# Performance work log

Measured on AMD Instinct MI355X. Metric: run time of the kernel, lower is better.

## Reference

```python
import jax, jax.numpy as jnp
import numpy as np

R = 4  # search_range

def setup_inputs() -> dict:
    key = jax.random.key(0)
    k1, k2 = jax.random.split(key)
    B, C, H, W = 4, 128, 96, 160
    src = jax.random.normal(k1, (B, C, H, W), dtype=jnp.float32)
    tgt = jax.random.normal(k2, (B, C, H, W), dtype=jnp.float32)
    return {"src": src, "tgt": tgt}

def _cost_volume(src, tgt):
    B, C, H, W = src.shape
    # zero-pad tgt by R on each spatial side (as in F.pad(tgt, [R]*4))
    tp = jnp.pad(tgt, ((0, 0), (0, 0), (R, R), (R, R)))
    # shifted map cropped to the central HxW window; shift (dh, dw) means
    # the neighbor at offset (dh, dw) relative to each src pixel.
    def crop(dh, dw):
        return tp[:, :, R + dh:R + dh + H, R + dw:R + dw + W]
    # order matches torch: [identity, left, right, up, down] for i=1..R
    maps = [crop(0, 0)]
    for i in range(1, R + 1):
        maps.extend([crop(-i, 0), crop(i, 0), crop(0, -i), crop(0, i)])
    neigh = jnp.stack(maps, axis=2)  # [B, C, 1+4R, H, W]
    # correlation: sum over channels -> [B, 1+4R, H, W]
    return jnp.einsum('bchw,bcshw->bshw', src, neigh)

def reference(src, tgt):
    return _cost_volume(src, tgt)
```

## Files before the change

### kernel.cpp

```cpp
#include <hip/hip_runtime.h>

#define RR 4
#define NS 17
#define BB 4
#define CC 128
#define HH 96
#define WW 160
#define HWSZ (HH * WW)

#define TW 32
#define HTILE 8
#define TROWS (HTILE + 2 * RR)
#define TCOLS (TW + 2 * RR)
#define TILE_E (TROWS * TCOLS)
#define CCHUNK 32
#define NCHUNK (CC / CCHUNK)
#define CG 8
#define NG (CCHUNK / CG)
#define NSPX (WW / TW)
#define NSPY (HH / HTILE)
#define NSP (NSPX * NSPY)
#define NWG (NSP * BB * NCHUNK)
#define NXCD 8
#define WGPX (NWG / NXCD)

#define FMA4S(a, t, s0, s1, s2, s3) \
    (a) = fmaf((s0), (t).x, fmaf((s1), (t).y, fmaf((s2), (t).z, fmaf((s3), (t).w, (a)))))

__global__ __launch_bounds__(256, 4)
void cost_volume_kernel(const float* __restrict__ src,
                        const float* __restrict__ tgt,
                        float* __restrict__ out) {
    __shared__ float4 tileA[TILE_E];
    __shared__ float4 tileB[TILE_E];

    const int x   = threadIdx.x;
    const int hg  = threadIdx.y;
    const int tid = hg * TW + x;

    const int flat = blockIdx.x;
    const int wg   = (flat & (NXCD - 1)) * WGPX + (flat >> 3);
    const int sp   = wg % NSP;
    const int z    = wg / NSP;
    const int wx   = sp % NSPX;
    const int wy   = sp / NSPX;

    const int w0 = wx * TW;
    const int h0 = wy * HTILE;
    const int b  = z & 3;
    const int c0 = (z >> 2) * CCHUNK;

    const int w = w0 + x;
    const int h = h0 + hg;

    const float* tgt_b = tgt + (size_t)(b * CC + c0) * HWSZ;
    const float* src_p = src + (size_t)(b * CC + c0) * HWSZ + h * WW + w;

    int  sOff[3];
    bool sVal[3];
#pragma unroll
    for (int k = 0; k < 3; ++k) {
        const int idx = tid + k * 256;
        const int r   = idx / TCOLS;
        const int col = idx - r * TCOLS;
        const int gr  = h0 - RR + r;
        const int gc  = w0 - RR + col;
        sVal[k] = (idx < TILE_E) && gr >= 0 && gr < HH && gc >= 0 && gc < WW;
        sOff[k] = gr * WW + gc;
    }

    float4 prA[3], prB[3];
    float  sv8[8];

    auto fetch = [&](int g) {
        const float* t = tgt_b + (size_t)(g * CG) * HWSZ;
#pragma unroll
        for (int k = 0; k < 3; ++k) {
            float4 va = make_float4(0.f, 0.f, 0.f, 0.f);
            float4 vb = make_float4(0.f, 0.f, 0.f, 0.f);
            if (sVal[k]) {
                const float* p = t + sOff[k];
                va.x = p[0];
                va.y = p[HWSZ];
                va.z = p[2 * HWSZ];
                va.w = p[3 * HWSZ];
                vb.x = p[4 * HWSZ];
                vb.y = p[5 * HWSZ];
                vb.z = p[6 * HWSZ];
                vb.w = p[7 * HWSZ];
            }
            prA[k] = va;
            prB[k] = vb;
        }
        const float* s = src_p + (size_t)(g * CG) * HWSZ;
#pragma unroll
        for (int k = 0; k < 8; ++k) sv8[k] = s[k * HWSZ];
    };

    float acc[NS];
#pragma unroll
    for (int s = 0; s < NS; ++s) acc[s] = 0.f;

    fetch(0);
    const int base = (RR + hg) * TCOLS + (RR + x);

    for (int g = 0; g < NG; ++g) {
        tileA[tid]       = prA[0];
        tileA[tid + 256] = prA[1];
        if (tid + 512 < TILE_E) tileA[tid + 512] = prA[2];
        tileB[tid]       = prB[0];
        tileB[tid + 256] = prB[1];
        if (tid + 512 < TILE_E) tileB[tid + 512] = prB[2];
        const float a0 = sv8[0], a1 = sv8[1], a2 = sv8[2], a3 = sv8[3];
        const float b0 = sv8[4], b1 = sv8[5], b2 = sv8[6], b3 = sv8[7];
        __syncthreads();

        if (g + 1 < NG) fetch(g + 1);

        {
            float4 tc = tileA[base];
            FMA4S(acc[0], tc, a0, a1, a2, a3);
#pragma unroll
            for (int off = 1; off <= RR; ++off) {
                float4 tu = tileA[base - off * TCOLS];
                float4 td = tileA[base + off * TCOLS];
                float4 tl = tileA[base - off];
                float4 tr = tileA[base + off];
                FMA4S(acc[4 * off - 3], tu, a0, a1, a2, a3);
                FMA4S(acc[4 * off - 2], td, a0, a1, a2, a3);
                FMA4S(acc[4 * off - 1], tl, a0, a1, a2, a3);
                FMA4S(acc[4 * off    ], tr, a0, a1, a2, a3);
            }
            float4 uc = tileB[base];
            FMA4S(acc[0], uc, b0, b1, b2, b3);
#pragma unroll
            for (int off = 1; off <= RR; ++off) {
                float4 tu = tileB[base - off * TCOLS];
                float4 td = tileB[base + off * TCOLS];
                float4 tl = tileB[base - off];
                float4 tr = tileB[base + off];
                FMA4S(acc[4 * off - 3], tu, b0, b1, b2, b3);
                FMA4S(acc[4 * off - 2], td, b0, b1, b2, b3);
                FMA4S(acc[4 * off - 1], tl, b0, b1, b2, b3);
                FMA4S(acc[4 * off    ], tr, b0, b1, b2, b3);
            }
        }
        __syncthreads();
    }

    float* op = out + (((size_t)b * NS) * HH + h) * WW + w;
#pragma unroll
    for (int s = 0; s < NS; ++s) {
        atomicAdd(op + (size_t)s * HWSZ, acc[s]);
    }
}

extern "C" void kernel_launch(void* const* d_in, const int* in_sizes, int n_in,
                              void* d_out, int out_size, void* d_ws, size_t ws_size,
                              hipStream_t stream) {
    const float* src = (const float*)d_in[0];
    const float* tgt = (const float*)d_in[1];
    float* out = (float*)d_out;

    hipMemsetAsync(out, 0, (size_t)out_size * sizeof(float), stream);

    dim3 block(TW, 8, 1);
    dim3 grid(NWG, 1, 1);
    cost_volume_kernel<<<grid, block, 0, stream>>>(src, tgt, out);
}
```

Baseline: 106.3 us.

## Split channel chunk across two half-blocks with in-LDS reduction to halve atomics

Doubles the channel chunk per workgroup to 64 and launches 512 threads, where each half of the block processes 32 channels in its own LDS tiles. The two halves' partial sums are combined through shared memory before one set of atomics is issued, so global atomic traffic is halved. This also drops the XCD-aware block remapping in favour of a simple channel-major ordering. LDS per block doubles and the grid halves, which may reduce occupancy and L2 locality.

```diff
diff --git a/kernel.cpp b/kernel.cpp
--- a/kernel.cpp
+++ b/kernel.cpp
@@ -13,42 +13,42 @@
 #define TROWS (HTILE + 2 * RR)
 #define TCOLS (TW + 2 * RR)
 #define TILE_E (TROWS * TCOLS)
-#define CCHUNK 32
+#define CCHUNK 64
 #define NCHUNK (CC / CCHUNK)
+#define CHALF (CCHUNK / 2)
 #define CG 8
-#define NG (CCHUNK / CG)
+#define NGH (CHALF / CG)
 #define NSPX (WW / TW)
 #define NSPY (HH / HTILE)
 #define NSP (NSPX * NSPY)
 #define NWG (NSP * BB * NCHUNK)
-#define NXCD 8
-#define WGPX (NWG / NXCD)
 
 #define FMA4S(a, t, s0, s1, s2, s3) \
     (a) = fmaf((s0), (t).x, fmaf((s1), (t).y, fmaf((s2), (t).z, fmaf((s3), (t).w, (a)))))
 
-__global__ __launch_bounds__(256, 4)
+__global__ __launch_bounds__(512, 4)
 void cost_volume_kernel(const float* __restrict__ src,
                         const float* __restrict__ tgt,
                         float* __restrict__ out) {
-    __shared__ float4 tileA[TILE_E];
-    __shared__ float4 tileB[TILE_E];
+    __shared__ float4 tile[2][2][TILE_E];
 
-    const int x   = threadIdx.x;
-    const int hg  = threadIdx.y;
-    const int tid = hg * TW + x;
+    const int x    = threadIdx.x;
+    const int yy   = threadIdx.y;
+    const int half = yy >> 3;
+    const int hg   = yy & 7;
+    const int tid  = hg * TW + x;
 
     const int flat = blockIdx.x;
-    const int wg   = (flat & (NXCD - 1)) * WGPX + (flat >> 3);
-    const int sp   = wg % NSP;
-    const int z    = wg / NSP;
-    const int wx   = sp % NSPX;
-    const int wy   = sp / NSPX;
+    const int ch64 = flat / 240;
+    const int rem  = flat % 240;
+    const int b    = rem / NSP;
+    const int spl  = rem % NSP;
+    const int wx   = spl % NSPX;
+    const int wy   = spl / NSPX;
 
+    const int c0 = ch64 * CCHUNK + half * CHALF;
     const int w0 = wx * TW;
     const int h0 = wy * HTILE;
-    const int b  = z & 3;
-    const int c0 = (z >> 2) * CCHUNK;
 
     const int w = w0 + x;
     const int h = h0 + hg;
@@ -103,42 +103,44 @@
 
     fetch(0);
     const int base = (RR + hg) * TCOLS + (RR + x);
+    float4* tA = tile[half][0];
+    float4* tB = tile[half][1];
 
-    for (int g = 0; g < NG; ++g) {
-        tileA[tid]       = prA[0];
-        tileA[tid + 256] = prA[1];
-        if (tid + 512 < TILE_E) tileA[tid + 512] = prA[2];
-        tileB[tid]       = prB[0];
-        tileB[tid + 256] = prB[1];
-        if (tid + 512 < TILE_E) tileB[tid + 512] = prB[2];
+    for (int g = 0; g < NGH; ++g) {
+        tA[tid]       = prA[0];
+        tA[tid + 256] = prA[1];
+        if (tid + 512 < TILE_E) tA[tid + 512] = prA[2];
+        tB[tid]       = prB[0];
+        tB[tid + 256] = prB[1];
+        if (tid + 512 < TILE_E) tB[tid + 512] = prB[2];
         const float a0 = sv8[0], a1 = sv8[1], a2 = sv8[2], a3 = sv8[3];
         const float b0 = sv8[4], b1 = sv8[5], b2 = sv8[6], b3 = sv8[7];
         __syncthreads();
 
-        if (g + 1 < NG) fetch(g + 1);
+        if (g + 1 < NGH) fetch(g + 1);
 
         {
-            float4 tc = tileA[base];
+            float4 tc = tA[base];
             FMA4S(acc[0], tc, a0, a1, a2, a3);
 #pragma unroll
             for (int off = 1; off <= RR; ++off) {
-                float4 tu = tileA[base - off * TCOLS];
-                float4 td = tileA[base + off * TCOLS];
-                float4 tl = tileA[base - off];
-                float4 tr = tileA[base + off];
+                float4 tu = tA[base - off * TCOLS];
+                float4 td = tA[base + off * TCOLS];
+                float4 tl = tA[base - off];
+                float4 tr = tA[base + off];
                 FMA4S(acc[4 * off - 3], tu, a0, a1, a2, a3);
                 FMA4S(acc[4 * off - 2], td, a0, a1, a2, a3);
                 FMA4S(acc[4 * off - 1], tl, a0, a1, a2, a3);
                 FMA4S(acc[4 * off    ], tr, a0, a1, a2, a3);
             }
-            float4 uc = tileB[base];
+            float4 uc = tB[base];
             FMA4S(acc[0], uc, b0, b1, b2, b3);
 #pragma unroll
             for (int off = 1; off <= RR; ++off) {
-                float4 tu = tileB[base - off * TCOLS];
-                float4 td = tileB[base + off * TCOLS];
-                float4 tl = tileB[base - off];
-                float4 tr = tileB[base + off];
+                float4 tu = tB[base - off * TCOLS];
+                float4 td = tB[base + off * TCOLS];
+                float4 tl = tB[base - off];
+                float4 tr = tB[base + off];
                 FMA4S(acc[4 * off - 3], tu, b0, b1, b2, b3);
                 FMA4S(acc[4 * off - 2], td, b0, b1, b2, b3);
                 FMA4S(acc[4 * off - 1], tl, b0, b1, b2, b3);
@@ -148,10 +150,18 @@
         __syncthreads();
     }
 
-    float* op = out + (((size_t)b * NS) * HH + h) * WW + w;
+    float* red = (float*)tile;
+    if (half) {
 #pragma unroll
-    for (int s = 0; s < NS; ++s) {
-        atomicAdd(op + (size_t)s * HWSZ, acc[s]);
+        for (int s = 0; s < NS; ++s) red[tid * NS + s] = acc[s];
+    }
+    __syncthreads();
+    if (!half) {
+        float* op = out + (((size_t)b * NS) * HH + h) * WW + w;
+#pragma unroll
+        for (int s = 0; s < NS; ++s) {
+            atomicAdd(op + (size_t)s * HWSZ, acc[s] + red[tid * NS + s]);
+        }
     }
 }
 
@@ -164,7 +174,7 @@
 
     hipMemsetAsync(out, 0, (size_t)out_size * sizeof(float), stream);
 
-    dim3 block(TW, 8, 1);
+    dim3 block(TW, 16, 1);
     dim3 grid(NWG, 1, 1);
     cost_volume_kernel<<<grid, block, 0, stream>>>(src, tgt, out);
 }
```

Result: slower. 112.1 us (+5.5%).
